# Optimization experiments

Measured on AMD Instinct MI355X. Metric: run time of the kernel, lower is better.

The kernel has to match this reference:

```python
import jax, jax.numpy as jnp
import numpy as np

T = 0.07          # cfg.CAP.TEMP
K = 50            # cfg.CAP.HARD_NEG_K
LOSS_WEIGHT = 0.5 # cfg.CAP.LOSS_WEIGHT
C_CAM = 8         # number of cameras
P = 2048          # pseudo-ID classes per camera bank


def setup_inputs() -> dict:
    key = jax.random.key(0)
    k1, k2, k3, k4 = jax.random.split(key, 4)
    B, D = 256, 2048
    inputs = jax.random.normal(k1, (B, D), jnp.float32)
    labels = jax.random.randint(k2, (B,), 0, P)
    cams = jax.random.randint(k3, (B,), 0, C_CAM)
    tempV = jax.random.normal(k4, (C_CAM * P, D), jnp.float32)
    tempV = tempV / jnp.linalg.norm(tempV, axis=1, keepdims=True)  # memory rows are L2-normalized
    return {"inputs": inputs, "labels": labels, "cams": cams, "tempV": tempV}


def _seg_mean_sum(vals, cams):
    # original loops over unique cams: loss += mean(vals within cam); empty cams contribute 0
    sums = jax.ops.segment_sum(vals, cams, num_segments=C_CAM)
    cnts = jax.ops.segment_sum(jnp.ones_like(vals), cams, num_segments=C_CAM)
    return jnp.sum(jnp.where(cnts > 0, sums / jnp.maximum(cnts, 1.0), 0.0))


def reference(inputs, labels, cams, tempV):
    B = inputs.shape[0]
    # cfg.CAP.NORM_FEAT
    x = inputs / jnp.linalg.norm(inputs, axis=1, keepdims=True)

    # one fused matmul against the concatenated memory; per-camera banks are contiguous P-slices
    all_logits = x @ tempV.T                      # [B, C_CAM*P]
    logits3 = all_logits.reshape(B, C_CAM, P)

    # ---- intra-camera loss: logits against the sample's own camera bank ----
    percam = jnp.take_along_axis(logits3, cams[:, None, None], axis=1)[:, 0, :] / T  # [B, P]
    lse_i = jax.scipy.special.logsumexp(percam, axis=1)
    ce = lse_i - jnp.take_along_axis(percam, labels[:, None], axis=1)[:, 0]
    loss_intra = _seg_mean_sum(ce, cams)

    # ---- inter-camera loss with hard-negative mining ----
    rows = jnp.arange(B)[:, None]
    # each ID has one centroid in every camera bank: positions label + P*cam
    ori_ind = labels[:, None] + P * jnp.arange(C_CAM)[None, :]        # [B, C_CAM]
    sims = all_logits.at[rows, ori_ind].set(-10000.0)                 # mask positives
    _, sel_ind = jax.lax.top_k(sims, K)                               # hard negatives (== sort[-K:])
    ori_logits = jnp.take_along_axis(all_logits, ori_ind, axis=1) / T  # [B, C_CAM]
    sel_logits = jnp.take_along_axis(all_logits, sel_ind, axis=1) / T  # [B, K]
    cat = jnp.concatenate([ori_logits, sel_logits], axis=1)            # [B, C_CAM+K]
    lse_c = jax.scipy.special.logsumexp(cat, axis=1)
    # target = 1/len(ori) on positives, 0 on negatives -> lse - mean(positive logits)
    loss_k = lse_c - jnp.mean(ori_logits, axis=1)
    loss_inter = LOSS_WEIGHT * _seg_mean_sum(loss_k, cams)

    return (loss_intra, loss_inter)
```

## Files before the change

kernel.cpp:

```cpp
#include <hip/hip_runtime.h>
#include <hip/hip_bf16.h>

#define BATCH 256
#define DIM   2048
#define NMEM  16384
#define PCLS  2048
#define CCAM  8
#define KSEL  50
#define T_INV 14.285714285714285714f
#define NBIN  4096

typedef __bf16 bf16x8 __attribute__((ext_vector_type(8)));
typedef float  f32x4  __attribute__((ext_vector_type(4)));

#define AS_GLOBAL __attribute__((address_space(1)))
#define AS_LDS    __attribute__((address_space(3)))

static __device__ __forceinline__ unsigned int f2bf(float f) {
  unsigned int u = __float_as_uint(f);
  return (u + 0x7FFFu + ((u >> 16) & 1u)) >> 16;
}
static __device__ __forceinline__ unsigned int pk2(float lo, float hi) {
  return f2bf(lo) | (f2bf(hi) << 16);
}
static __device__ __forceinline__ int binof(float v) {
  float bf = fmaf(v, 1950.4762f, 2048.0f);
  bf = fminf(fmaxf(bf, 0.0f), 4095.0f);
  return (int)bf;
}

__global__ __launch_bounds__(256) void norm_cast_kernel(
    const float* __restrict__ in, unsigned short* __restrict__ xb) {
  __shared__ float red[256];
  const int b = blockIdx.x, t = threadIdx.x;
  const float4* row = (const float4*)(in + (size_t)b * DIM);
  float4 a0 = row[t];
  float4 a1 = row[t + 256];
  float ss = a0.x*a0.x + a0.y*a0.y + a0.z*a0.z + a0.w*a0.w
           + a1.x*a1.x + a1.y*a1.y + a1.z*a1.z + a1.w*a1.w;
  red[t] = ss; __syncthreads();
  for (int s = 128; s > 0; s >>= 1) { if (t < s) red[t] += red[t + s]; __syncthreads(); }
  const float rn = rsqrtf(red[0]);
  ushort4 o0, o1;
  o0.x = (unsigned short)f2bf(a0.x*rn); o0.y = (unsigned short)f2bf(a0.y*rn);
  o0.z = (unsigned short)f2bf(a0.z*rn); o0.w = (unsigned short)f2bf(a0.w*rn);
  o1.x = (unsigned short)f2bf(a1.x*rn); o1.y = (unsigned short)f2bf(a1.y*rn);
  o1.z = (unsigned short)f2bf(a1.z*rn); o1.w = (unsigned short)f2bf(a1.w*rn);
  *(ushort4*)&xb[(size_t)b * DIM + t * 4]         = o0;
  *(ushort4*)&xb[(size_t)b * DIM + (t + 256) * 4] = o1;
}

#define BM 128
#define BN 64
#define BK 64
#define NT (DIM / BK)

__global__ __launch_bounds__(256, 2) void gemm_kernel(
    const unsigned short* __restrict__ X,
    const float* __restrict__ V,
    float* __restrict__ C) {
  __shared__ __align__(16) unsigned short As[2][BM * BK];
  __shared__ __align__(16) float          Bs[2][BN * BK];
  const int t  = threadIdx.x;
  const int m0 = blockIdx.x * BM;
  const int n0 = blockIdx.y * BN;
  const int lane = t & 63;
  const int w    = t >> 6;
  const int wm   = (w >> 1) * 64;
  const int wn   = (w & 1) * 32;
  const int fr   = lane & 15;
  const int fko  = lane >> 4;

  f32x4 acc[4][2];
#pragma unroll
  for (int i = 0; i < 4; i++)
#pragma unroll
    for (int j = 0; j < 2; j++) acc[i][j] = (f32x4){0.f, 0.f, 0.f, 0.f};

  const unsigned short* Abase =
      X + (size_t)(m0 + w * 32 + (lane >> 3)) * DIM + ((lane & 7) ^ (lane >> 3)) * 8;
  const float* Bbase = V + (size_t)(n0 + w * 16 + (lane >> 4)) * DIM;
  const int cB = (lane & 15) ^ (lane >> 4);

  auto glds_tile = [&](int buf, int k0) {
#pragma unroll
    for (int q = 0; q < 4; q++) {
      __builtin_amdgcn_global_load_lds(
          (const AS_GLOBAL unsigned int*)(Abase + (size_t)q * 8 * DIM + k0),
          (AS_LDS unsigned int*)&As[buf][(w * 32 + q * 8) * BK],
          16, 0, 0);
    }
#pragma unroll
    for (int q = 0; q < 4; q++) {
      const int c = cB ^ (q * 4);
      __builtin_amdgcn_global_load_lds(
          (const AS_GLOBAL unsigned int*)(Bbase + (size_t)q * 4 * DIM + k0 + c * 4),
          (AS_LDS unsigned int*)&Bs[buf][(w * 16 + q * 4) * BK],
          16, 0, 0);
    }
  };

  auto compute = [&](int buf) {
#pragma unroll
    for (int kk = 0; kk < BK; kk += 32) {
      bf16x8 aF[4], bF[2];
#pragma unroll
      for (int i = 0; i < 4; i++) {
        const int R  = wm + i * 16 + fr;
        const int c0 = (kk >> 3) + fko;
        const int p  = c0 ^ (fr & 7);
        aF[i] = *(const bf16x8*)&As[buf][R * BK + p * 8];
      }
#pragma unroll
      for (int j = 0; j < 2; j++) {
        const int RN = wn + j * 16 + fr;
        const int c0 = (kk + fko * 8) >> 2;
        const int p0 = c0 ^ fr, p1 = (c0 + 1) ^ fr;
        const float4* Brow = (const float4*)&Bs[buf][RN * BK];
        const float4 lo = Brow[p0];
        const float4 hi = Brow[p1];
        uint4 pk;
        pk.x = pk2(lo.x, lo.y); pk.y = pk2(lo.z, lo.w);
        pk.z = pk2(hi.x, hi.y); pk.w = pk2(hi.z, hi.w);
        bF[j] = *(bf16x8*)&pk;
      }
#pragma unroll
      for (int i = 0; i < 4; i++)
#pragma unroll
        for (int j = 0; j < 2; j++)
          acc[i][j] = __builtin_amdgcn_mfma_f32_16x16x32_bf16(aF[i], bF[j], acc[i][j], 0, 0, 0);
    }
  };

  glds_tile(0, 0);
  __syncthreads();

  for (int kt = 0; kt < NT; kt += 2) {
    if (kt + 1 < NT) glds_tile(1, (kt + 1) * BK);
    compute(0);
    __syncthreads();
    if (kt + 2 < NT) glds_tile(0, (kt + 2) * BK);
    compute(1);
    __syncthreads();
  }

  const int cr = (lane >> 4) * 4;
  const int cc = lane & 15;
#pragma unroll
  for (int i = 0; i < 4; i++)
#pragma unroll
    for (int j = 0; j < 2; j++)
#pragma unroll
      for (int r = 0; r < 4; r++)
        C[(size_t)(m0 + wm + i * 16 + cr + r) * NMEM + (n0 + wn + j * 16 + cc)] =
            acc[i][j][r];
}

__global__ __launch_bounds__(256) void row_loss_kernel(
    const float* __restrict__ logits,
    const int* __restrict__ labels, const int* __restrict__ cams,
    float* __restrict__ ce_out, float* __restrict__ lossk_out) {
  __shared__ float vals[NMEM];
  __shared__ int   hist[NBIN];
  __shared__ float red[256];
  __shared__ int   pint[256];
  __shared__ float bl[512];
  __shared__ int   bcount;
  __shared__ int   bstar_s, cabove_s;

  const int b = blockIdx.x, t = threadIdx.x;
  const float4* src = (const float4*)(logits + (size_t)b * NMEM);
#pragma unroll
  for (int i = 0; i < 16; i++) ((float4*)vals)[t + 256 * i] = src[t + 256 * i];
#pragma unroll
  for (int i = 0; i < NBIN / 256; i++) hist[t + 256 * i] = 0;
  if (t == 0) bcount = 0;
  const int cam = cams[b], label = labels[b];
  __syncthreads();

  const int s0 = cam * PCLS;
  float S = 0.f;
#pragma unroll
  for (int i = 0; i < 8; i++) S += __expf(vals[s0 + t + 256 * i] * T_INV);
  red[t] = S; __syncthreads();
  for (int s = 128; s > 0; s >>= 1) { if (t < s) red[t] += red[t + s]; __syncthreads(); }
  float ov[CCAM]; float sumo = 0.f;
  if (t == 0) {
    ce_out[b] = logf(red[0]) - vals[s0 + label] * T_INV;
#pragma unroll
    for (int c = 0; c < CCAM; c++) { ov[c] = vals[c * PCLS + label]; sumo += ov[c]; }
  }
  __syncthreads();
  if (t < CCAM) vals[t * PCLS + label] = -1e30f;
  __syncthreads();

#pragma unroll
  for (int i = 0; i < 64; i++) {
    int bin = binof(vals[t + 256 * i]);
    atomicAdd(&hist[bin], 1);
  }
  __syncthreads();

  int ps = 0;
#pragma unroll
  for (int i = 0; i < 16; i++) ps += hist[t * 16 + i];
  pint[t] = ps; __syncthreads();
  if (t == 0) {
    int cum = 0, bstar = 0, cab = 0;
    for (int tc = 255; tc >= 0; tc--) {
      if (cum + pint[tc] >= KSEL) {
        for (int bi = tc * 16 + 15; bi >= tc * 16; bi--) {
          int h = hist[bi];
          if (cum + h >= KSEL) { bstar = bi; cab = cum; break; }
          cum += h;
        }
        break;
      }
      cum += pint[tc];
    }
    bstar_s = bstar; cabove_s = cab;
  }
  __syncthreads();
  const int bstar = bstar_s;

  float S2 = 0.f;
#pragma unroll
  for (int i = 0; i < 64; i++) {
    float v = vals[t + 256 * i];
    int bin = binof(v);
    if (bin > bstar) S2 += __expf(v * T_INV);
    else if (bin == bstar) {
      int p = atomicAdd(&bcount, 1);
      if (p < 512) bl[p] = v;
    }
  }
  red[t] = S2; __syncthreads();
  for (int s = 128; s > 0; s >>= 1) { if (t < s) red[t] += red[t + s]; __syncthreads(); }

  if (t == 0) {
    float S2tot = red[0];
    int need = KSEL - cabove_s;
    int bc = min(bcount, 512);
    for (int r = 0; r < need; r++) {
      float mx = -1e30f; int mi = 0;
      for (int i = 0; i < bc; i++) if (bl[i] > mx) { mx = bl[i]; mi = i; }
      S2tot += __expf(mx * T_INV);
      bl[mi] = -1e30f;
    }
#pragma unroll
    for (int c = 0; c < CCAM; c++) S2tot += __expf(ov[c] * T_INV);
    lossk_out[b] = logf(S2tot) - (sumo * T_INV) * (1.0f / CCAM);
  }
}

__global__ __launch_bounds__(256) void finalize_kernel(
    const float* __restrict__ ce, const float* __restrict__ lossk,
    const int* __restrict__ cams, float* __restrict__ out) {
  __shared__ float ce_s[BATCH], lk_s[BATCH];
  __shared__ int   cam_s[BATCH];
  __shared__ float si[CCAM], sk[CCAM], cnt[CCAM];
  const int t = threadIdx.x;
  ce_s[t]  = ce[t];
  lk_s[t]  = lossk[t];
  cam_s[t] = cams[t];
  __syncthreads();
  if (t < CCAM) {
    float a = 0.f, b = 0.f; int n = 0;
    for (int i = 0; i < BATCH; i++) {
      if (cam_s[i] == t) { a += ce_s[i]; b += lk_s[i]; n++; }
    }
    si[t] = a; sk[t] = b; cnt[t] = (float)n;
  }
  __syncthreads();
  if (t == 0) {
    float li = 0.f, lk = 0.f;
    for (int c = 0; c < CCAM; c++) {
      if (cnt[c] > 0.f) { li += si[c] / cnt[c]; lk += sk[c] / cnt[c]; }
    }
    out[0] = li;
    out[1] = 0.5f * lk;
  }
}

extern "C" void kernel_launch(void* const* d_in, const int* in_sizes, int n_in,
                              void* d_out, int out_size, void* d_ws, size_t ws_size,
                              hipStream_t stream) {
  const float* inputs = (const float*)d_in[0];
  const int*   labels = (const int*)d_in[1];
  const int*   cams   = (const int*)d_in[2];
  const float* tempV  = (const float*)d_in[3];
  float* out = (float*)d_out;

  char* ws = (char*)d_ws;
  unsigned short* xb  = (unsigned short*)ws;
  float* logits       = (float*)(ws + (1u << 20));
  float* ce           = (float*)(ws + (1u << 20) + (16u << 20));
  float* lossk        = (float*)(ws + (1u << 20) + (16u << 20) + 1024);

  norm_cast_kernel<<<BATCH, 256, 0, stream>>>(inputs, xb);
  gemm_kernel<<<dim3(BATCH / BM, NMEM / BN), 256, 0, stream>>>(xb, tempV, logits);
  row_loss_kernel<<<BATCH, 256, 0, stream>>>(logits, labels, cams, ce, lossk);
  finalize_kernel<<<1, 256, 0, stream>>>(ce, lossk, cams, out);
}
```

Measured before the change: 275.5 us.

## Split GEMM K dimension in two with atomic accumulation and single LDS buffer

The GEMM grid gains a z-dimension of 2, so each block covers half of the K range and adds its partial result into a zeroed logits buffer with atomic adds. A memset is added before the GEMM. The LDS double buffer is replaced by a single buffer with a sync after load and after compute, and launch bounds are raised to 4 blocks per CU. The aim is more blocks and higher occupancy, at the cost of losing load/compute overlap inside a block, an extra 16 MB memset, and atomic traffic on the output.

Result: no change. 275.3 us (-0.1%).

```diff
diff --git a/kernel.cpp b/kernel.cpp
--- a/kernel.cpp
+++ b/kernel.cpp
@@ -53,17 +53,19 @@
 #define BM 128
 #define BN 64
 #define BK 64
-#define NT (DIM / BK)
-
-__global__ __launch_bounds__(256, 2) void gemm_kernel(
+#define KHALF (DIM / 2)
+#define NTH   (KHALF / BK)
+
+__global__ __launch_bounds__(256, 4) void gemm_kernel(
     const unsigned short* __restrict__ X,
     const float* __restrict__ V,
     float* __restrict__ C) {
-  __shared__ __align__(16) unsigned short As[2][BM * BK];
-  __shared__ __align__(16) float          Bs[2][BN * BK];
+  __shared__ __align__(16) unsigned short As[BM * BK];
+  __shared__ __align__(16) float          Bs[BN * BK];
   const int t  = threadIdx.x;
   const int m0 = blockIdx.x * BM;
   const int n0 = blockIdx.y * BN;
+  const int kb = blockIdx.z * KHALF;
   const int lane = t & 63;
   const int w    = t >> 6;
   const int wm   = (w >> 1) * 64;
@@ -78,16 +80,18 @@
     for (int j = 0; j < 2; j++) acc[i][j] = (f32x4){0.f, 0.f, 0.f, 0.f};
 
   const unsigned short* Abase =
-      X + (size_t)(m0 + w * 32 + (lane >> 3)) * DIM + ((lane & 7) ^ (lane >> 3)) * 8;
-  const float* Bbase = V + (size_t)(n0 + w * 16 + (lane >> 4)) * DIM;
+      X + (size_t)(m0 + w * 32 + (lane >> 3)) * DIM + kb
+        + ((lane & 7) ^ (lane >> 3)) * 8;
+  const float* Bbase = V + (size_t)(n0 + w * 16 + (lane >> 4)) * DIM + kb;
   const int cB = (lane & 15) ^ (lane >> 4);
 
-  auto glds_tile = [&](int buf, int k0) {
+  for (int kt = 0; kt < NTH; kt++) {
+    const int k0 = kt * BK;
 #pragma unroll
     for (int q = 0; q < 4; q++) {
       __builtin_amdgcn_global_load_lds(
           (const AS_GLOBAL unsigned int*)(Abase + (size_t)q * 8 * DIM + k0),
-          (AS_LDS unsigned int*)&As[buf][(w * 32 + q * 8) * BK],
+          (AS_LDS unsigned int*)&As[(w * 32 + q * 8) * BK],
           16, 0, 0);
     }
 #pragma unroll
@@ -95,12 +99,11 @@
       const int c = cB ^ (q * 4);
       __builtin_amdgcn_global_load_lds(
           (const AS_GLOBAL unsigned int*)(Bbase + (size_t)q * 4 * DIM + k0 + c * 4),
-          (AS_LDS unsigned int*)&Bs[buf][(w * 16 + q * 4) * BK],
+          (AS_LDS unsigned int*)&Bs[(w * 16 + q * 4) * BK],
           16, 0, 0);
     }
-  };
-
-  auto compute = [&](int buf) {
+    __syncthreads();
+
 #pragma unroll
     for (int kk = 0; kk < BK; kk += 32) {
       bf16x8 aF[4], bF[2];
@@ -109,14 +112,14 @@
         const int R  = wm + i * 16 + fr;
         const int c0 = (kk >> 3) + fko;
         const int p  = c0 ^ (fr & 7);
-        aF[i] = *(const bf16x8*)&As[buf][R * BK + p * 8];
+        aF[i] = *(const bf16x8*)&As[R * BK + p * 8];
       }
 #pragma unroll
       for (int j = 0; j < 2; j++) {
         const int RN = wn + j * 16 + fr;
         const int c0 = (kk + fko * 8) >> 2;
         const int p0 = c0 ^ fr, p1 = (c0 + 1) ^ fr;
-        const float4* Brow = (const float4*)&Bs[buf][RN * BK];
+        const float4* Brow = (const float4*)&Bs[RN * BK];
         const float4 lo = Brow[p0];
         const float4 hi = Brow[p1];
         uint4 pk;
@@ -130,17 +133,6 @@
         for (int j = 0; j < 2; j++)
           acc[i][j] = __builtin_amdgcn_mfma_f32_16x16x32_bf16(aF[i], bF[j], acc[i][j], 0, 0, 0);
     }
-  };
-
-  glds_tile(0, 0);
-  __syncthreads();
-
-  for (int kt = 0; kt < NT; kt += 2) {
-    if (kt + 1 < NT) glds_tile(1, (kt + 1) * BK);
-    compute(0);
-    __syncthreads();
-    if (kt + 2 < NT) glds_tile(0, (kt + 2) * BK);
-    compute(1);
     __syncthreads();
   }
 
@@ -152,8 +144,9 @@
     for (int j = 0; j < 2; j++)
 #pragma unroll
       for (int r = 0; r < 4; r++)
-        C[(size_t)(m0 + wm + i * 16 + cr + r) * NMEM + (n0 + wn + j * 16 + cc)] =
-            acc[i][j][r];
+        unsafeAtomicAdd(
+            &C[(size_t)(m0 + wm + i * 16 + cr + r) * NMEM + (n0 + wn + j * 16 + cc)],
+            acc[i][j][r]);
 }
 
 __global__ __launch_bounds__(256) void row_loss_kernel(
@@ -298,7 +291,8 @@
   float* lossk        = (float*)(ws + (1u << 20) + (16u << 20) + 1024);
 
   norm_cast_kernel<<<BATCH, 256, 0, stream>>>(inputs, xb);
-  gemm_kernel<<<dim3(BATCH / BM, NMEM / BN), 256, 0, stream>>>(xb, tempV, logits);
+  hipMemsetAsync(logits, 0, (size_t)BATCH * NMEM * sizeof(float), stream);
+  gemm_kernel<<<dim3(BATCH / BM, NMEM / BN, 2), 256, 0, stream>>>(xb, tempV, logits);
   row_loss_kernel<<<BATCH, 256, 0, stream>>>(logits, labels, cams, ce, lossk);
   finalize_kernel<<<1, 256, 0, stream>>>(ce, lossk, cams, out);
 }
```
